# Kernel tuning notes

Hardware: AMD Instinct MI355X
Metric: run time of the kernel (lower is better)

The kernel has to match this reference:

```python
import jax, jax.numpy as jnp
import numpy as np

DIM = 1024
NUM_HEADS = 16
HEAD_DIM = DIM // NUM_HEADS
SCALE = HEAD_DIM ** -0.5


def setup_inputs() -> dict:
    key = jax.random.key(0)
    ks = jax.random.split(key, 11)
    B, T = 2, 2048
    std = DIM ** -0.5
    return {
        "query": jax.random.normal(ks[0], (B, T, DIM), jnp.float32),
        "key": jax.random.normal(ks[1], (B, T, DIM), jnp.float32),
        "value": jax.random.normal(ks[2], (B, T, DIM), jnp.float32),
        "wq": jax.random.normal(ks[3], (DIM, DIM), jnp.float32) * std,
        "bq": jnp.zeros((DIM,), jnp.float32),
        "wk": jax.random.normal(ks[4], (DIM, DIM), jnp.float32) * std,
        "bk": jnp.zeros((DIM,), jnp.float32),
        "wv": jax.random.normal(ks[5], (DIM, DIM), jnp.float32) * std,
        "bv": jnp.zeros((DIM,), jnp.float32),
        "wo": jax.random.normal(ks[6], (DIM, DIM), jnp.float32) * std,
        "bo": jnp.zeros((DIM,), jnp.float32),
    }


def reference(query, key, value, wq, bq, wk, bk, wv, bv, wo, bo):
    B, Tq, D = query.shape
    Tk = key.shape[1]
    H, Hd = NUM_HEADS, HEAD_DIM
    # projections (torch Linear: x @ W^T + b); reshape to [B, H, T, Hd]
    q = (query @ wq.T + bq).reshape(B, Tq, H, Hd).transpose(0, 2, 1, 3)
    k = (key @ wk.T + bk).reshape(B, Tk, H, Hd).transpose(0, 2, 1, 3)
    v = (value @ wv.T + bv).reshape(B, Tk, H, Hd).transpose(0, 2, 1, 3)
    # attention scores [B, H, Tq, Tk]
    attn = jnp.einsum("bhqd,bhkd->bhqk", q, k) * SCALE
    attn = jax.nn.softmax(attn, axis=-1)
    # dropout p=0.0 -> identity
    out = jnp.einsum("bhqk,bhkd->bhqd", attn, v)
    out = out.transpose(0, 2, 1, 3).reshape(B, Tq, D)
    return out @ wo.T + bo
```

## Files before the change

### kernel.cpp

```cpp
#include <hip/hip_runtime.h>
#include <math.h>


typedef __attribute__((ext_vector_type(8))) short short8;
typedef __attribute__((ext_vector_type(4))) float f32x4;
typedef __attribute__((ext_vector_type(4))) float float4v;
typedef __attribute__((ext_vector_type(4))) unsigned short ushort4v;
typedef __attribute__((ext_vector_type(2))) unsigned int uint2v;

typedef __attribute__((address_space(3))) unsigned int lds_uint;
typedef __attribute__((address_space(1))) unsigned int glb_uint;

__device__ __forceinline__ void gload_lds16(const void* g, void* l) {
    __builtin_amdgcn_global_load_lds((glb_uint*)(unsigned long long)g,
                                     (lds_uint*)(unsigned int)(unsigned long long)l,
                                     16, 0, 0);
}

__device__ __forceinline__ unsigned short f32_bf16(float f) {
    union { float f; unsigned int u; } x; x.f = f;
    unsigned int r = x.u + 0x7fffu + ((x.u >> 16) & 1u);
    return (unsigned short)(r >> 16);
}

__device__ __forceinline__ unsigned int cvt_pk_bf16(float lo, float hi) {
    unsigned int r;
    asm("v_cvt_pk_bf16_f32 %0, %1, %2" : "=v"(r) : "v"(lo), "v"(hi));
    return r;
}

__device__ __forceinline__ float exp2_fast(float x) {
    float r;
    asm("v_exp_f32 %0, %1" : "=v"(r) : "v"(x));
    return r;
}

#define QSCALE 0.18033688011112042f

__global__ void pack3_bf16(const float* __restrict__ a, const float* __restrict__ b,
                           const float* __restrict__ c,
                           unsigned short* __restrict__ oa, unsigned short* __restrict__ ob,
                           unsigned short* __restrict__ oc, int n4) {
    const int y = blockIdx.y;
    const float* in = (y == 0) ? a : (y == 1) ? b : c;
    unsigned short* out = (y == 0) ? oa : (y == 1) ? ob : oc;
    int i = blockIdx.x * blockDim.x + threadIdx.x;
    if (i < n4) {
        float4v v = ((const float4v*)in)[i];
        ushort4v o;
        o.x = f32_bf16(v.x); o.y = f32_bf16(v.y);
        o.z = f32_bf16(v.z); o.w = f32_bf16(v.w);
        ((ushort4v*)out)[i] = o;
    }
}

__global__ void pack4_bf16(const float* __restrict__ a, const float* __restrict__ b,
                           const float* __restrict__ c, const float* __restrict__ d,
                           unsigned short* __restrict__ oa, unsigned short* __restrict__ ob,
                           unsigned short* __restrict__ oc, unsigned short* __restrict__ od,
                           int n4) {
    const int y = blockIdx.y;
    const float* in = (y == 0) ? a : (y == 1) ? b : (y == 2) ? c : d;
    unsigned short* out = (y == 0) ? oa : (y == 1) ? ob : (y == 2) ? oc : od;
    int i = blockIdx.x * blockDim.x + threadIdx.x;
    if (i < n4) {
        float4v v = ((const float4v*)in)[i];
        ushort4v o;
        o.x = f32_bf16(v.x); o.y = f32_bf16(v.y);
        o.z = f32_bf16(v.z); o.w = f32_bf16(v.w);
        ((ushort4v*)out)[i] = o;
    }
}

__global__ __launch_bounds__(256, 2) void gemm_qkv(
    const unsigned short* __restrict__ A0, const unsigned short* __restrict__ A1,
    const unsigned short* __restrict__ A2,
    const unsigned short* __restrict__ W0, const unsigned short* __restrict__ W1,
    const unsigned short* __restrict__ W2,
    const float* __restrict__ bs0, const float* __restrict__ bs1,
    const float* __restrict__ bs2,
    unsigned short* __restrict__ O0, unsigned short* __restrict__ O1,
    unsigned short* __restrict__ O2)
{
    const int z = blockIdx.z;
    const unsigned short* A = (z == 0) ? A0 : (z == 1) ? A1 : A2;
    const unsigned short* W = (z == 0) ? W0 : (z == 1) ? W1 : W2;
    const float* bias        = (z == 0) ? bs0 : (z == 1) ? bs1 : bs2;
    unsigned short* C        = (z == 0) ? O0 : (z == 1) ? O1 : O2;
    const float oscale = (z == 0) ? QSCALE : 1.0f;
    const int N = 1024, K = 1024;

    __shared__ unsigned short As[128 * 64];
    __shared__ unsigned short Bs[128 * 64];
    const int tid  = threadIdx.x;
    const int lane = tid & 63, wave = tid >> 6;
    const int l15 = lane & 15, l4 = lane >> 4;
    const int bm = blockIdx.y * 128, bn = blockIdx.x * 128;
    const int wr = wave >> 1, wc = wave & 1;
    const int swz = l15 & 7;

    f32x4 acc[4][4];
    #pragma unroll
    for (int i = 0; i < 4; ++i)
        #pragma unroll
        for (int j = 0; j < 4; ++j)
            #pragma unroll
            for (int e = 0; e < 4; ++e) acc[i][j][e] = 0.f;

    const int srow = lane >> 3;
    const int scol = ((lane & 7) ^ srow) * 8;

    for (int k0 = 0; k0 < K; k0 += 64) {
        __syncthreads();
        #pragma unroll
        for (int i = 0; i < 4; ++i) {
            int c = wave * 4 + i;
            int row = c * 8 + srow;
            gload_lds16(A + (size_t)(bm + row) * K + k0 + scol, &As[c * 512]);
            gload_lds16(W + (size_t)(bn + row) * K + k0 + scol, &Bs[c * 512]);
        }
        __syncthreads();
        #pragma unroll
        for (int kk = 0; kk < 2; ++kk) {
            short8 af[4], bf[4];
            const int ko = ((kk * 4 + l4) ^ swz) << 3;
            #pragma unroll
            for (int i = 0; i < 4; ++i)
                af[i] = *(const short8*)&As[(wr * 64 + i * 16 + l15) * 64 + ko];
            #pragma unroll
            for (int j = 0; j < 4; ++j)
                bf[j] = *(const short8*)&Bs[(wc * 64 + j * 16 + l15) * 64 + ko];
            #pragma unroll
            for (int i = 0; i < 4; ++i)
                #pragma unroll
                for (int j = 0; j < 4; ++j)
                    acc[i][j] = __builtin_amdgcn_mfma_f32_16x16x32_bf16(
                        af[i], bf[j], acc[i][j], 0, 0, 0);
        }
    }

    #pragma unroll
    for (int j = 0; j < 4; ++j) {
        const int col = bn + wc * 64 + j * 16 + l15;
        const float bj = bias[col];
        #pragma unroll
        for (int i = 0; i < 4; ++i) {
            const int row0 = bm + wr * 64 + i * 16 + l4 * 4;
            #pragma unroll
            for (int r = 0; r < 4; ++r) {
                const int row = row0 + r;
                const float v = (acc[i][j][r] + bj) * oscale;
                if (z < 2) {
                    C[(size_t)row * N + col] = f32_bf16(v);
                } else {
                    const int b = row >> 11, t = row & 2047;
                    C[(((size_t)((b << 4) + (col >> 6)) * 64
                        + (col & 63)) << 11) + t] = f32_bf16(v);
                }
            }
        }
    }
}

__global__ __launch_bounds__(256, 3) void gemm_out(
    const unsigned short* __restrict__ A,
    const unsigned short* __restrict__ W,
    const float* __restrict__ bias,
    float* __restrict__ C)
{
    const int N = 1024, K = 1024;
    __shared__ unsigned short As[2][64 * 64];
    __shared__ unsigned short Bs[2][128 * 64];
    const int tid  = threadIdx.x;
    const int lane = tid & 63, wave = tid >> 6;
    const int l15 = lane & 15, l4 = lane >> 4;
    const int bm = blockIdx.y * 64, bn = blockIdx.x * 128;
    const int wr = wave >> 1, wc = wave & 1;
    const int swz = l15 & 7;

    f32x4 acc[2][4];
    #pragma unroll
    for (int i = 0; i < 2; ++i)
        #pragma unroll
        for (int j = 0; j < 4; ++j)
            #pragma unroll
            for (int e = 0; e < 4; ++e) acc[i][j][e] = 0.f;

    const int srow = lane >> 3;
    const int scol = ((lane & 7) ^ srow) * 8;

    auto stage = [&](int bf, int k0) {
        #pragma unroll
        for (int i = 0; i < 2; ++i) {
            const int c = wave * 2 + i;
            gload_lds16(A + (size_t)(bm + c * 8 + srow) * K + k0 + scol,
                        &As[bf][c * 512]);
        }
        #pragma unroll
        for (int i = 0; i < 4; ++i) {
            const int c = wave * 4 + i;
            gload_lds16(W + (size_t)(bn + c * 8 + srow) * K + k0 + scol,
                        &Bs[bf][c * 512]);
        }
    };

    stage(0, 0);
    __syncthreads();

    int bufi = 0;
    for (int k0 = 0; k0 < K; k0 += 64) {
        if (k0 + 64 < K) stage(bufi ^ 1, k0 + 64);
        #pragma unroll
        for (int kk = 0; kk < 2; ++kk) {
            short8 af[2], bf[4];
            const int ko = ((kk * 4 + l4) ^ swz) << 3;
            #pragma unroll
            for (int i = 0; i < 2; ++i)
                af[i] = *(const short8*)&As[bufi][(wr * 32 + i * 16 + l15) * 64 + ko];
            #pragma unroll
            for (int j = 0; j < 4; ++j)
                bf[j] = *(const short8*)&Bs[bufi][(wc * 64 + j * 16 + l15) * 64 + ko];
            #pragma unroll
            for (int i = 0; i < 2; ++i)
                #pragma unroll
                for (int j = 0; j < 4; ++j)
                    acc[i][j] = __builtin_amdgcn_mfma_f32_16x16x32_bf16(
                        af[i], bf[j], acc[i][j], 0, 0, 0);
        }
        __syncthreads();
        bufi ^= 1;
    }

    #pragma unroll
    for (int j = 0; j < 4; ++j) {
        const int col = bn + wc * 64 + j * 16 + l15;
        const float bj = bias[col];
        #pragma unroll
        for (int i = 0; i < 2; ++i) {
            const int row0 = bm + wr * 32 + i * 16 + l4 * 4;
            #pragma unroll
            for (int r = 0; r < 4; ++r)
                C[(size_t)(row0 + r) * N + col] = acc[i][j][r] + bj;
        }
    }
}

__global__ __launch_bounds__(512, 4) void attn_fwd(
    const unsigned short* __restrict__ qp,
    const unsigned short* __restrict__ kp,
    const unsigned short* __restrict__ vt,
    unsigned short* __restrict__ op)
{
    __shared__ unsigned short Ks[2][64 * 64];
    __shared__ unsigned short Vs[2][64 * 64];
    __shared__ unsigned short P[8][16 * 64];

    const int tid = threadIdx.x;
    const int lane = tid & 63, wave = tid >> 6;
    const int l15 = lane & 15, l4 = lane >> 4;
    const int swz = (l15 & 7) << 3;

    const int flat = blockIdx.x;
    const int swzb = (flat & 7) * 64 + (flat >> 3);
    const int bx = swzb & 15;
    const int bh = swzb >> 4;
    const int b = bh >> 4, h = bh & 15;
    const int q0 = bx * 128 + wave * 16;

    const size_t xbase = (size_t)b * 2048 * 1024 + h * 64;
    const size_t vbase = (size_t)bh * 64 * 2048;

    const int sr = lane >> 3;
    const int sc = ((lane & 7) ^ sr) * 8;

    short8 bq[2];
    #pragma unroll
    for (int kk = 0; kk < 2; ++kk)
        bq[kk] = *(const short8*)&qp[xbase
            + (size_t)(q0 + l15) * 1024 + kk * 32 + l4 * 8];

    f32x4 acc[4];
    #pragma unroll
    for (int dj = 0; dj < 4; ++dj)
        #pragma unroll
        for (int e = 0; e < 4; ++e) acc[dj][e] = 0.f;

    float m_run = -1e30f, l_run = 0.f;

    {
        const int c = wave;
        gload_lds16(kp + xbase + (size_t)(c * 8 + sr) * 1024 + sc,
                    &Ks[0][c * 512]);
        gload_lds16(vt + vbase + (size_t)(c * 8 + sr) * 2048 + sc,
                    &Vs[0][c * 512]);
    }
    __syncthreads();

    const int NT = 2048 / 64;
    int buf = 0;
    for (int t = 0; t < NT; ++t) {
        const int kv0 = t * 64;
        if (t + 1 < NT) {
            const int c = wave;
            gload_lds16(kp + xbase + (size_t)(kv0 + 64 + c * 8 + sr) * 1024 + sc,
                        &Ks[buf ^ 1][c * 512]);
            gload_lds16(vt + vbase + (size_t)(c * 8 + sr) * 2048 + kv0 + 64 + sc,
                        &Vs[buf ^ 1][c * 512]);
        }

        f32x4 st[4];
        {
            short8 ak[4];
            #pragma unroll
            for (int j = 0; j < 4; ++j)
                ak[j] = *(const short8*)&Ks[buf][(j * 16 + l15) * 64
                                                 + ((l4 << 3) ^ swz)];
            const f32x4 z4 = {0.f, 0.f, 0.f, 0.f};
            #pragma unroll
            for (int j = 0; j < 4; ++j)
                st[j] = __builtin_amdgcn_mfma_f32_16x16x32_bf16(
                    ak[j], bq[0], z4, 0, 0, 0);
            #pragma unroll
            for (int j = 0; j < 4; ++j)
                ak[j] = *(const short8*)&Ks[buf][(j * 16 + l15) * 64
                                                 + (((4 + l4) << 3) ^ swz)];
            #pragma unroll
            for (int j = 0; j < 4; ++j)
                st[j] = __builtin_amdgcn_mfma_f32_16x16x32_bf16(
                    ak[j], bq[1], st[j], 0, 0, 0);
        }

        short8 av[2][4];
        #pragma unroll
        for (int kvc = 0; kvc < 2; ++kvc)
            #pragma unroll
            for (int dj = 0; dj < 4; ++dj)
                av[kvc][dj] = *(const short8*)&Vs[buf][(dj * 16 + l15) * 64
                                                 + (((kvc * 4 + l4) << 3) ^ swz)];

        {
            float tm[4];
            #pragma unroll
            for (int j = 0; j < 4; ++j)
                tm[j] = fmaxf(fmaxf(st[j][0], st[j][1]),
                              fmaxf(st[j][2], st[j][3]));
            float mx = fmaxf(fmaxf(tm[0], tm[1]), fmaxf(tm[2], tm[3]));
            mx = fmaxf(mx, __shfl_xor(mx, 16));
            mx = fmaxf(mx, __shfl_xor(mx, 32));
            const float mnew = fmaxf(m_run, mx);
            const float corr = exp2_fast(m_run - mnew);
            m_run = mnew;
            float ts[4];
            #pragma unroll
            for (int j = 0; j < 4; ++j) {
                float p0 = exp2_fast(st[j][0] - mnew);
                float p1 = exp2_fast(st[j][1] - mnew);
                float p2 = exp2_fast(st[j][2] - mnew);
                float p3 = exp2_fast(st[j][3] - mnew);
                st[j][0] = p0; st[j][1] = p1; st[j][2] = p2; st[j][3] = p3;
                ts[j] = (p0 + p1) + (p2 + p3);
            }
            float ls = (ts[0] + ts[1]) + (ts[2] + ts[3]);
            ls += __shfl_xor(ls, 16);
            ls += __shfl_xor(ls, 32);
            l_run = l_run * corr + ls;
            #pragma unroll
            for (int dj = 0; dj < 4; ++dj) acc[dj] *= corr;
        }

        #pragma unroll
        for (int j = 0; j < 4; ++j) {
            uint2v w;
            w.x = cvt_pk_bf16(st[j][0], st[j][1]);
            w.y = cvt_pk_bf16(st[j][2], st[j][3]);
            *(uint2v*)&P[wave][l15 * 64 + ((j * 16 + l4 * 4) ^ swz)] = w;
        }

        #pragma unroll
        for (int kvc = 0; kvc < 2; ++kvc) {
            short8 pb = *(const short8*)&P[wave][l15 * 64
                                                + (((kvc * 4 + l4) << 3) ^ swz)];
            #pragma unroll
            for (int dj = 0; dj < 4; ++dj)
                acc[dj] = __builtin_amdgcn_mfma_f32_16x16x32_bf16(
                    av[kvc][dj], pb, acc[dj], 0, 0, 0);
        }

        __syncthreads();
        buf ^= 1;
    }

    {
        const float inv = 1.0f / l_run;
        const int t = q0 + l15;
        #pragma unroll
        for (int dj = 0; dj < 4; ++dj) {
            uint2v w;
            w.x = cvt_pk_bf16(acc[dj][0] * inv, acc[dj][1] * inv);
            w.y = cvt_pk_bf16(acc[dj][2] * inv, acc[dj][3] * inv);
            *(uint2v*)&op[((size_t)(b * 2048 + t)) * 1024
                          + h * 64 + dj * 16 + l4 * 4] = w;
        }
    }
}

extern "C" void kernel_launch(void* const* d_in, const int* in_sizes, int n_in,
                              void* d_out, int out_size, void* d_ws, size_t ws_size,
                              hipStream_t stream)
{
    const float* q  = (const float*)d_in[0];
    const float* k  = (const float*)d_in[1];
    const float* v  = (const float*)d_in[2];
    const float* wq = (const float*)d_in[3];
    const float* bq = (const float*)d_in[4];
    const float* wk = (const float*)d_in[5];
    const float* bk = (const float*)d_in[6];
    const float* wv = (const float*)d_in[7];
    const float* bv = (const float*)d_in[8];
    const float* wo = (const float*)d_in[9];
    const float* bo = (const float*)d_in[10];
    float* out = (float*)d_out;

    const int M = 4096, N = 1024, K = 1024;
    unsigned char* ws = (unsigned char*)d_ws;
    const size_t SX = (size_t)M * K * 2;
    const size_t SW = (size_t)N * K * 2;
    unsigned short* xq  = (unsigned short*)(ws);
    unsigned short* xk  = (unsigned short*)(ws + SX);
    unsigned short* xv  = (unsigned short*)(ws + 2 * SX);
    unsigned short* wqb = (unsigned short*)(ws + 3 * SX);
    unsigned short* wkb = (unsigned short*)(ws + 3 * SX + SW);
    unsigned short* wvb = (unsigned short*)(ws + 3 * SX + 2 * SW);
    unsigned short* wob = (unsigned short*)(ws + 3 * SX + 3 * SW);
    unsigned short* qp  = (unsigned short*)(ws + 3 * SX + 4 * SW);
    unsigned short* kp  = qp + (size_t)M * N;
    unsigned short* vt  = kp + (size_t)M * N;
    unsigned short* opb = vt + (size_t)M * N;

    pack3_bf16<<<dim3(4096, 3), 256, 0, stream>>>(q, k, v, xq, xk, xv,
                                                  M * K / 4);
    pack4_bf16<<<dim3(1024, 4), 256, 0, stream>>>(wq, wk, wv, wo,
                                                  wqb, wkb, wvb, wob, N * K / 4);

    gemm_qkv<<<dim3(8, 32, 3), 256, 0, stream>>>(xq, xk, xv, wqb, wkb, wvb,
                                                 bq, bk, bv, qp, kp, vt);

    attn_fwd<<<dim3(512), 512, 0, stream>>>(qp, kp, vt, opb);

    gemm_out<<<dim3(8, 64), 256, 0, stream>>>(opb, wob, bo, out);
}
```

Measured before the change: 131.4 us.

## Use 128-wide KV tiles per barrier and defer row-sum shuffle reduction

The attention kernel now stages 128 keys per pipeline step, split into two 64-key halves processed inside one iteration. This halves the number of __syncthreads barriers and staging rounds. The per-tile cross-lane reduction of the softmax row sum is replaced by a per-lane partial sum that is reduced once in the epilogue. Shared memory per block doubles for the K/V buffers, which may reduce occupancy under the 4-blocks-per-CU launch bound.

```diff
diff --git a/kernel.cpp b/kernel.cpp
--- a/kernel.cpp
+++ b/kernel.cpp
@@ -251,8 +251,8 @@
     const unsigned short* __restrict__ vt,
     unsigned short* __restrict__ op)
 {
-    __shared__ unsigned short Ks[2][64 * 64];
-    __shared__ unsigned short Vs[2][64 * 64];
+    __shared__ unsigned short Ks[2][128 * 64];
+    __shared__ unsigned short Vs[2][2][64 * 64];
     __shared__ unsigned short P[8][16 * 64];
 
     const int tid = threadIdx.x;
@@ -285,105 +285,108 @@
         #pragma unroll
         for (int e = 0; e < 4; ++e) acc[dj][e] = 0.f;
 
-    float m_run = -1e30f, l_run = 0.f;
-
-    {
-        const int c = wave;
-        gload_lds16(kp + xbase + (size_t)(c * 8 + sr) * 1024 + sc,
-                    &Ks[0][c * 512]);
-        gload_lds16(vt + vbase + (size_t)(c * 8 + sr) * 2048 + sc,
-                    &Vs[0][c * 512]);
-    }
+    float m_run = -1e30f, l_part = 0.f;
+
+    auto stage = [&](int bf, int kv0) {
+        #pragma unroll
+        for (int i = 0; i < 2; ++i) {
+            const int c = wave * 2 + i;
+            gload_lds16(kp + xbase + (size_t)(kv0 + c * 8 + sr) * 1024 + sc,
+                        &Ks[bf][c * 512]);
+        }
+        #pragma unroll
+        for (int h2 = 0; h2 < 2; ++h2)
+            gload_lds16(vt + vbase + (size_t)(wave * 8 + sr) * 2048
+                            + kv0 + h2 * 64 + sc,
+                        &Vs[bf][h2][wave * 512]);
+    };
+
+    stage(0, 0);
     __syncthreads();
 
-    const int NT = 2048 / 64;
+    const int NT = 2048 / 128;
     int buf = 0;
     for (int t = 0; t < NT; ++t) {
-        const int kv0 = t * 64;
-        if (t + 1 < NT) {
-            const int c = wave;
-            gload_lds16(kp + xbase + (size_t)(kv0 + 64 + c * 8 + sr) * 1024 + sc,
-                        &Ks[buf ^ 1][c * 512]);
-            gload_lds16(vt + vbase + (size_t)(c * 8 + sr) * 2048 + kv0 + 64 + sc,
-                        &Vs[buf ^ 1][c * 512]);
-        }
-
-        f32x4 st[4];
-        {
-            short8 ak[4];
-            #pragma unroll
-            for (int j = 0; j < 4; ++j)
-                ak[j] = *(const short8*)&Ks[buf][(j * 16 + l15) * 64
-                                                 + ((l4 << 3) ^ swz)];
-            const f32x4 z4 = {0.f, 0.f, 0.f, 0.f};
-            #pragma unroll
-            for (int j = 0; j < 4; ++j)
-                st[j] = __builtin_amdgcn_mfma_f32_16x16x32_bf16(
-                    ak[j], bq[0], z4, 0, 0, 0);
-            #pragma unroll
-            for (int j = 0; j < 4; ++j)
-                ak[j] = *(const short8*)&Ks[buf][(j * 16 + l15) * 64
-                                                 + (((4 + l4) << 3) ^ swz)];
-            #pragma unroll
-            for (int j = 0; j < 4; ++j)
-                st[j] = __builtin_amdgcn_mfma_f32_16x16x32_bf16(
-                    ak[j], bq[1], st[j], 0, 0, 0);
-        }
-
-        short8 av[2][4];
-        #pragma unroll
-        for (int kvc = 0; kvc < 2; ++kvc)
-            #pragma unroll
-            for (int dj = 0; dj < 4; ++dj)
-                av[kvc][dj] = *(const short8*)&Vs[buf][(dj * 16 + l15) * 64
-                                                 + (((kvc * 4 + l4) << 3) ^ swz)];
-
-        {
-            float tm[4];
-            #pragma unroll
-            for (int j = 0; j < 4; ++j)
-                tm[j] = fmaxf(fmaxf(st[j][0], st[j][1]),
-                              fmaxf(st[j][2], st[j][3]));
-            float mx = fmaxf(fmaxf(tm[0], tm[1]), fmaxf(tm[2], tm[3]));
-            mx = fmaxf(mx, __shfl_xor(mx, 16));
-            mx = fmaxf(mx, __shfl_xor(mx, 32));
-            const float mnew = fmaxf(m_run, mx);
-            const float corr = exp2_fast(m_run - mnew);
-            m_run = mnew;
-            float ts[4];
+        if (t + 1 < NT) stage(buf ^ 1, (t + 1) * 128);
+
+        #pragma unroll
+        for (int hh = 0; hh < 2; ++hh) {
+            f32x4 st[4];
+            {
+                short8 ak[4];
+                #pragma unroll
+                for (int j = 0; j < 4; ++j)
+                    ak[j] = *(const short8*)&Ks[buf][(hh * 64 + j * 16 + l15) * 64
+                                                     + ((l4 << 3) ^ swz)];
+                const f32x4 z4 = {0.f, 0.f, 0.f, 0.f};
+                #pragma unroll
+                for (int j = 0; j < 4; ++j)
+                    st[j] = __builtin_amdgcn_mfma_f32_16x16x32_bf16(
+                        ak[j], bq[0], z4, 0, 0, 0);
+                #pragma unroll
+                for (int j = 0; j < 4; ++j)
+                    ak[j] = *(const short8*)&Ks[buf][(hh * 64 + j * 16 + l15) * 64
+                                                     + (((4 + l4) << 3) ^ swz)];
+                #pragma unroll
+                for (int j = 0; j < 4; ++j)
+                    st[j] = __builtin_amdgcn_mfma_f32_16x16x32_bf16(
+                        ak[j], bq[1], st[j], 0, 0, 0);
+            }
+
+            short8 av[2][4];
+            #pragma unroll
+            for (int kvc = 0; kvc < 2; ++kvc)
+                #pragma unroll
+                for (int dj = 0; dj < 4; ++dj)
+                    av[kvc][dj] = *(const short8*)&Vs[buf][hh]
+                        [(dj * 16 + l15) * 64 + (((kvc * 4 + l4) << 3) ^ swz)];
+
+            {
+                float tm[4];
+                #pragma unroll
+                for (int j = 0; j < 4; ++j)
+                    tm[j] = fmaxf(fmaxf(st[j][0], st[j][1]),
+                                  fmaxf(st[j][2], st[j][3]));
+                float mx = fmaxf(fmaxf(tm[0], tm[1]), fmaxf(tm[2], tm[3]));
+                mx = fmaxf(mx, __shfl_xor(mx, 16));
+                mx = fmaxf(mx, __shfl_xor(mx, 32));
+                const float mnew = fmaxf(m_run, mx);
+                const float corr = exp2_fast(m_run - mnew);
+                m_run = mnew;
+                float ts[4];
+                #pragma unroll
+                for (int j = 0; j < 4; ++j) {
+                    float p0 = exp2_fast(st[j][0] - mnew);
+                    float p1 = exp2_fast(st[j][1] - mnew);
+                    float p2 = exp2_fast(st[j][2] - mnew);
+                    float p3 = exp2_fast(st[j][3] - mnew);
+                    st[j][0] = p0; st[j][1] = p1;
+                    st[j][2] = p2; st[j][3] = p3;
+                    ts[j] = (p0 + p1) + (p2 + p3);
+                }
+                l_part = l_part * corr
+                         + ((ts[0] + ts[1]) + (ts[2] + ts[3]));
+                #pragma unroll
+                for (int dj = 0; dj < 4; ++dj) acc[dj] *= corr;
+            }
+
             #pragma unroll
             for (int j = 0; j < 4; ++j) {
-                float p0 = exp2_fast(st[j][0] - mnew);
-                float p1 = exp2_fast(st[j][1] - mnew);
-                float p2 = exp2_fast(st[j][2] - mnew);
-                float p3 = exp2_fast(st[j][3] - mnew);
-                st[j][0] = p0; st[j][1] = p1; st[j][2] = p2; st[j][3] = p3;
-                ts[j] = (p0 + p1) + (p2 + p3);
+                uint2v w;
+                w.x = cvt_pk_bf16(st[j][0], st[j][1]);
+                w.y = cvt_pk_bf16(st[j][2], st[j][3]);
+                *(uint2v*)&P[wave][l15 * 64 + ((j * 16 + l4 * 4) ^ swz)] = w;
             }
-            float ls = (ts[0] + ts[1]) + (ts[2] + ts[3]);
-            ls += __shfl_xor(ls, 16);
-            ls += __shfl_xor(ls, 32);
-            l_run = l_run * corr + ls;
-            #pragma unroll
-            for (int dj = 0; dj < 4; ++dj) acc[dj] *= corr;
-        }
-
-        #pragma unroll
-        for (int j = 0; j < 4; ++j) {
-            uint2v w;
-            w.x = cvt_pk_bf16(st[j][0], st[j][1]);
-            w.y = cvt_pk_bf16(st[j][2], st[j][3]);
-            *(uint2v*)&P[wave][l15 * 64 + ((j * 16 + l4 * 4) ^ swz)] = w;
-        }
-
-        #pragma unroll
-        for (int kvc = 0; kvc < 2; ++kvc) {
-            short8 pb = *(const short8*)&P[wave][l15 * 64
+
+            #pragma unroll
+            for (int kvc = 0; kvc < 2; ++kvc) {
+                short8 pb = *(const short8*)&P[wave][l15 * 64
                                                 + (((kvc * 4 + l4) << 3) ^ swz)];
-            #pragma unroll
-            for (int dj = 0; dj < 4; ++dj)
-                acc[dj] = __builtin_amdgcn_mfma_f32_16x16x32_bf16(
-                    av[kvc][dj], pb, acc[dj], 0, 0, 0);
+                #pragma unroll
+                for (int dj = 0; dj < 4; ++dj)
+                    acc[dj] = __builtin_amdgcn_mfma_f32_16x16x32_bf16(
+                        av[kvc][dj], pb, acc[dj], 0, 0, 0);
+            }
         }
 
         __syncthreads();
@@ -391,7 +394,10 @@
     }
 
     {
-        const float inv = 1.0f / l_run;
+        float l = l_part;
+        l += __shfl_xor(l, 16);
+        l += __shfl_xor(l, 32);
+        const float inv = 1.0f / l;
         const int t = q0 + l15;
         #pragma unroll
         for (int dj = 0; dj < 4; ++dj) {
```

Measured after the change: 130.0 us. No clear change (-1.0%).

## Split attention KV range in two with partial outputs and a combine kernel

Applied to the files above, without the earlier changes.

The attention kernel now splits each head's KV sequence into two halves. This doubles the grid from 512 to 1024 blocks and raises launch bounds occupancy from 4 to 8. Each half writes unnormalised bf16 partial accumulators plus its running max and sum into reused workspace, and a new combine kernel merges the two halves. K/V double buffering was dropped to single buffers with two syncs per tile to cut LDS use. The trade-offs are lost load/compute overlap, an extra launch and memory round trip, and bf16 rounding of the unnormalised partials.

```diff
diff --git a/kernel.cpp b/kernel.cpp
--- a/kernel.cpp
+++ b/kernel.cpp
@@ -21,6 +21,11 @@
     union { float f; unsigned int u; } x; x.f = f;
     unsigned int r = x.u + 0x7fffu + ((x.u >> 16) & 1u);
     return (unsigned short)(r >> 16);
+}
+
+__device__ __forceinline__ float bf16_f32(unsigned short u) {
+    union { unsigned int i; float f; } x; x.i = ((unsigned int)u) << 16;
+    return x.f;
 }
 
 __device__ __forceinline__ unsigned int cvt_pk_bf16(float lo, float hi) {
@@ -245,14 +250,15 @@
     }
 }
 
-__global__ __launch_bounds__(512, 4) void attn_fwd(
+__global__ __launch_bounds__(512, 8) void attn_fwd(
     const unsigned short* __restrict__ qp,
     const unsigned short* __restrict__ kp,
     const unsigned short* __restrict__ vt,
-    unsigned short* __restrict__ op)
+    unsigned short* __restrict__ pacc,
+    float* __restrict__ pml)
 {
-    __shared__ unsigned short Ks[2][64 * 64];
-    __shared__ unsigned short Vs[2][64 * 64];
+    __shared__ unsigned short Ks[64 * 64];
+    __shared__ unsigned short Vs[64 * 64];
     __shared__ unsigned short P[8][16 * 64];
 
     const int tid = threadIdx.x;
@@ -261,11 +267,14 @@
     const int swz = (l15 & 7) << 3;
 
     const int flat = blockIdx.x;
-    const int swzb = (flat & 7) * 64 + (flat >> 3);
-    const int bx = swzb & 15;
-    const int bh = swzb >> 4;
+    const int swzb = (flat & 7) * 128 + (flat >> 3);
+    const int qtile = swzb & 15;
+    const int rest = swzb >> 4;
+    const int bh = rest & 31;
+    const int kvh = rest >> 5;
     const int b = bh >> 4, h = bh & 15;
-    const int q0 = bx * 128 + wave * 16;
+    const int q0 = qtile * 128 + wave * 16;
+    const int kvbase = kvh * 1024;
 
     const size_t xbase = (size_t)b * 2048 * 1024 + h * 64;
     const size_t vbase = (size_t)bh * 64 * 2048;
@@ -285,36 +294,28 @@
         #pragma unroll
         for (int e = 0; e < 4; ++e) acc[dj][e] = 0.f;
 
-    float m_run = -1e30f, l_run = 0.f;
-
-    {
-        const int c = wave;
-        gload_lds16(kp + xbase + (size_t)(c * 8 + sr) * 1024 + sc,
-                    &Ks[0][c * 512]);
-        gload_lds16(vt + vbase + (size_t)(c * 8 + sr) * 2048 + sc,
-                    &Vs[0][c * 512]);
-    }
-    __syncthreads();
-
-    const int NT = 2048 / 64;
-    int buf = 0;
+    float m_run = -1e30f, l_part = 0.f;
+
+    const int NT = 16;
     for (int t = 0; t < NT; ++t) {
-        const int kv0 = t * 64;
-        if (t + 1 < NT) {
+        const int kv0 = kvbase + t * 64;
+        __syncthreads();
+        {
             const int c = wave;
-            gload_lds16(kp + xbase + (size_t)(kv0 + 64 + c * 8 + sr) * 1024 + sc,
-                        &Ks[buf ^ 1][c * 512]);
-            gload_lds16(vt + vbase + (size_t)(c * 8 + sr) * 2048 + kv0 + 64 + sc,
-                        &Vs[buf ^ 1][c * 512]);
-        }
+            gload_lds16(kp + xbase + (size_t)(kv0 + c * 8 + sr) * 1024 + sc,
+                        &Ks[c * 512]);
+            gload_lds16(vt + vbase + (size_t)(c * 8 + sr) * 2048 + kv0 + sc,
+                        &Vs[c * 512]);
+        }
+        __syncthreads();
 
         f32x4 st[4];
         {
             short8 ak[4];
             #pragma unroll
             for (int j = 0; j < 4; ++j)
-                ak[j] = *(const short8*)&Ks[buf][(j * 16 + l15) * 64
-                                                 + ((l4 << 3) ^ swz)];
+                ak[j] = *(const short8*)&Ks[(j * 16 + l15) * 64
+                                            + ((l4 << 3) ^ swz)];
             const f32x4 z4 = {0.f, 0.f, 0.f, 0.f};
             #pragma unroll
             for (int j = 0; j < 4; ++j)
@@ -322,8 +323,8 @@
                     ak[j], bq[0], z4, 0, 0, 0);
             #pragma unroll
             for (int j = 0; j < 4; ++j)
-                ak[j] = *(const short8*)&Ks[buf][(j * 16 + l15) * 64
-                                                 + (((4 + l4) << 3) ^ swz)];
+                ak[j] = *(const short8*)&Ks[(j * 16 + l15) * 64
+                                            + (((4 + l4) << 3) ^ swz)];
             #pragma unroll
             for (int j = 0; j < 4; ++j)
                 st[j] = __builtin_amdgcn_mfma_f32_16x16x32_bf16(
@@ -335,8 +336,8 @@
         for (int kvc = 0; kvc < 2; ++kvc)
             #pragma unroll
             for (int dj = 0; dj < 4; ++dj)
-                av[kvc][dj] = *(const short8*)&Vs[buf][(dj * 16 + l15) * 64
-                                                 + (((kvc * 4 + l4) << 3) ^ swz)];
+                av[kvc][dj] = *(const short8*)&Vs[(dj * 16 + l15) * 64
+                                            + (((kvc * 4 + l4) << 3) ^ swz)];
 
         {
             float tm[4];
@@ -360,10 +361,7 @@
                 st[j][0] = p0; st[j][1] = p1; st[j][2] = p2; st[j][3] = p3;
                 ts[j] = (p0 + p1) + (p2 + p3);
             }
-            float ls = (ts[0] + ts[1]) + (ts[2] + ts[3]);
-            ls += __shfl_xor(ls, 16);
-            ls += __shfl_xor(ls, 32);
-            l_run = l_run * corr + ls;
+            l_part = l_part * corr + ((ts[0] + ts[1]) + (ts[2] + ts[3]));
             #pragma unroll
             for (int dj = 0; dj < 4; ++dj) acc[dj] *= corr;
         }
@@ -379,29 +377,60 @@
         #pragma unroll
         for (int kvc = 0; kvc < 2; ++kvc) {
             short8 pb = *(const short8*)&P[wave][l15 * 64
-                                                + (((kvc * 4 + l4) << 3) ^ swz)];
+                                            + (((kvc * 4 + l4) << 3) ^ swz)];
             #pragma unroll
             for (int dj = 0; dj < 4; ++dj)
                 acc[dj] = __builtin_amdgcn_mfma_f32_16x16x32_bf16(
                     av[kvc][dj], pb, acc[dj], 0, 0, 0);
         }
-
-        __syncthreads();
-        buf ^= 1;
     }
 
     {
-        const float inv = 1.0f / l_run;
-        const int t = q0 + l15;
+        float l = l_part;
+        l += __shfl_xor(l, 16);
+        l += __shfl_xor(l, 32);
+        const size_t row = (size_t)bh * 2048 + q0 + l15;
+        const size_t base = ((size_t)kvh * 65536 + row) * 64;
         #pragma unroll
         for (int dj = 0; dj < 4; ++dj) {
             uint2v w;
-            w.x = cvt_pk_bf16(acc[dj][0] * inv, acc[dj][1] * inv);
-            w.y = cvt_pk_bf16(acc[dj][2] * inv, acc[dj][3] * inv);
-            *(uint2v*)&op[((size_t)(b * 2048 + t)) * 1024
-                          + h * 64 + dj * 16 + l4 * 4] = w;
-        }
-    }
+            w.x = cvt_pk_bf16(acc[dj][0], acc[dj][1]);
+            w.y = cvt_pk_bf16(acc[dj][2], acc[dj][3]);
+            *(uint2v*)&pacc[base + dj * 16 + l4 * 4] = w;
+        }
+        if (l4 == 0) {
+            const size_t mi = ((size_t)kvh * 65536 + row) * 2;
+            pml[mi]     = m_run;
+            pml[mi + 1] = l;
+        }
+    }
+}
+
+__global__ void attn_combine(const unsigned short* __restrict__ pacc,
+                             const float* __restrict__ pml,
+                             unsigned short* __restrict__ op)
+{
+    const int tid = threadIdx.x;
+    const int rl = tid >> 4;
+    const int dl = (tid & 15) * 4;
+    const size_t row = (size_t)blockIdx.x * 16 + rl;
+    const float m0 = pml[row * 2], l0 = pml[row * 2 + 1];
+    const float m1 = pml[(65536 + row) * 2], l1 = pml[(65536 + row) * 2 + 1];
+    const float mm = fmaxf(m0, m1);
+    const float s0 = exp2_fast(m0 - mm), s1 = exp2_fast(m1 - mm);
+    const float inv = 1.0f / (l0 * s0 + l1 * s1);
+    const ushort4v a0 = *(const ushort4v*)&pacc[row * 64 + dl];
+    const ushort4v a1 = *(const ushort4v*)&pacc[(65536ull + row) * 64 + dl];
+    float o[4];
+    #pragma unroll
+    for (int e = 0; e < 4; ++e)
+        o[e] = (bf16_f32(a0[e]) * s0 + bf16_f32(a1[e]) * s1) * inv;
+    const int bh = (int)(row >> 11), t = (int)(row & 2047);
+    const int b = bh >> 4, h = bh & 15;
+    uint2v w;
+    w.x = cvt_pk_bf16(o[0], o[1]);
+    w.y = cvt_pk_bf16(o[2], o[3]);
+    *(uint2v*)&op[((size_t)(b * 2048 + t)) * 1024 + h * 64 + dl] = w;
 }
 
 extern "C" void kernel_launch(void* const* d_in, const int* in_sizes, int n_in,
@@ -437,6 +466,9 @@
     unsigned short* vt  = kp + (size_t)M * N;
     unsigned short* opb = vt + (size_t)M * N;
 
+    unsigned short* pacc = xq;
+    float*          pml  = (float*)xv;
+
     pack3_bf16<<<dim3(4096, 3), 256, 0, stream>>>(q, k, v, xq, xk, xv,
                                                   M * K / 4);
     pack4_bf16<<<dim3(1024, 4), 256, 0, stream>>>(wq, wk, wv, wo,
@@ -445,7 +477,8 @@
     gemm_qkv<<<dim3(8, 32, 3), 256, 0, stream>>>(xq, xk, xv, wqb, wkb, wvb,
                                                  bq, bk, bv, qp, kp, vt);
 
-    attn_fwd<<<dim3(512), 512, 0, stream>>>(qp, kp, vt, opb);
+    attn_fwd<<<dim3(1024), 512, 0, stream>>>(qp, kp, vt, pacc, pml);
+    attn_combine<<<dim3(4096), 256, 0, stream>>>(pacc, pml, opb);
 
     gemm_out<<<dim3(8, 64), 256, 0, stream>>>(opb, wob, bo, out);
 }
```

After: 143.4 us. +9.1%, slower.
